# Performance work log

Measured on AMD Instinct MI355X. Metric: run time of the kernel, lower is better.

Reference implementation:

```python
import jax, jax.numpy as jnp
import numpy as np

D_MODEL, D_INNER, D_STATE, DT_RANK, D_CONV = 768, 1536, 16, 48, 4
B, L = 2, 2048


def setup_inputs() -> dict:
    key = jax.random.key(0)
    ks = jax.random.split(key, 8)
    s = 0.02
    return {
        "x": jax.random.normal(ks[0], (B, L, D_MODEL), jnp.float32),
        "norm_w": jnp.ones((D_MODEL,), jnp.float32),
        "in_proj_w": jax.random.normal(ks[1], (2 * D_INNER, D_MODEL), jnp.float32) * s,
        "conv_w": jax.random.normal(ks[2], (D_INNER, 1, D_CONV), jnp.float32) * s,
        "conv_b": jnp.zeros((D_INNER,), jnp.float32),
        "x_proj_w": jax.random.normal(ks[3], (DT_RANK + 2 * D_STATE, D_INNER), jnp.float32) * s,
        "dt_proj_w": jax.random.normal(ks[4], (D_INNER, DT_RANK), jnp.float32) * s,
        "dt_proj_b": jax.random.normal(ks[5], (D_INNER,), jnp.float32) * s,
        "A_log": jnp.broadcast_to(jnp.log(jnp.arange(1, D_STATE + 1, dtype=jnp.float32)), (D_INNER, D_STATE)).copy(),
        "D": jnp.ones((D_INNER,), jnp.float32),
        "out_proj_w": jax.random.normal(ks[6], (D_MODEL, D_INNER), jnp.float32) * s,
    }


def _mamba_block(x, norm_w, in_proj_w, conv_w, conv_b, x_proj_w,
                 dt_proj_w, dt_proj_b, A_log, D, out_proj_w):
    residual = x
    # RMSNorm
    h = x * jax.lax.rsqrt(jnp.mean(x * x, axis=-1, keepdims=True) + 1e-5) * norm_w
    # in_proj -> chunk into (hs, gate)
    xz = jnp.einsum('bld,ed->ble', h, in_proj_w)          # [B,L,2*Di]
    xh, z = jnp.split(xz, 2, axis=-1)                     # each [B,L,Di]
    # causal depthwise conv1d (kernel D_CONV) + SiLU
    xt = jnp.transpose(xh, (0, 2, 1))                     # [B,Di,L]
    xt = jnp.pad(xt, ((0, 0), (0, 0), (D_CONV - 1, 0)))
    xc = jax.lax.conv_general_dilated(xt, conv_w, (1,), 'VALID',
                                      feature_group_count=D_INNER)
    xc = jax.nn.silu(xc + conv_b[None, :, None])
    xc = jnp.transpose(xc, (0, 2, 1))                     # [B,L,Di]
    # x_proj -> (dt, B, C)
    proj = jnp.einsum('bld,ed->ble', xc, x_proj_w)        # [B,L,dt_rank+2N]
    dt, Bm, Cm = jnp.split(proj, [DT_RANK, DT_RANK + D_STATE], axis=-1)
    delta = jax.nn.softplus(jnp.einsum('blr,dr->bld', dt, dt_proj_w) + dt_proj_b)  # [B,L,Di]
    A = -jnp.exp(A_log)                                   # [Di,N]
    dA = jnp.exp(delta[..., None] * A)                    # [B,L,Di,N]
    dBx = delta[..., None] * Bm[:, :, None, :] * xc[..., None]  # [B,L,Di,N]
    # selective scan over the sequence axis
    def step(hst, inp):
        dA_t, dBx_t, C_t = inp                            # [B,Di,N],[B,Di,N],[B,N]
        hst = dA_t * hst + dBx_t
        y = jnp.einsum('bdn,bn->bd', hst, C_t)
        return hst, y
    h0 = jnp.zeros((x.shape[0], D_INNER, D_STATE), x.dtype)
    _, ys = jax.lax.scan(step, h0, (jnp.moveaxis(dA, 1, 0),
                                    jnp.moveaxis(dBx, 1, 0),
                                    jnp.moveaxis(Cm, 1, 0)))
    y = jnp.moveaxis(ys, 0, 1)                            # [B,L,Di]
    y = y + xc * D                                        # skip connection D
    y = y * jax.nn.silu(z)                                # gate
    out = jnp.einsum('bld,ed->ble', y, out_proj_w)        # [B,L,Dm]
    return residual + out, residual


def reference(x, norm_w, in_proj_w, conv_w, conv_b, x_proj_w,
              dt_proj_w, dt_proj_b, A_log, D, out_proj_w):
    return _mamba_block(x, norm_w, in_proj_w, conv_w, conv_b, x_proj_w,
                        dt_proj_w, dt_proj_b, A_log, D, out_proj_w)
```

## Files before the change

kernel.cpp:

```cpp
#include <hip/hip_runtime.h>
#include <cstdint>
#include <cstddef>

typedef __bf16 bf16_t;
typedef __bf16 bf16x8 __attribute__((ext_vector_type(8)));
typedef float  f32x4  __attribute__((ext_vector_type(4)));

#define D_MODEL 768
#define D_INNER 1536
#define D_STATE 16
#define DT_RANK 48
#define NB      2
#define SEQ     2048
#define NTOK    (NB*SEQ)
#define XPROJ_N (DT_RANK + 2*D_STATE)
#define LC      32
#define NCHUNK  (SEQ/LC)
#define XP_KS   4
#define XP_KC   (D_INNER/XP_KS)

#define N_INW (2*D_INNER*D_MODEL)
#define N_XPW (XPROJ_N*D_INNER)
#define N_DTW (D_INNER*DT_RANK)
#define N_OPW (D_MODEL*D_INNER)
#define N_CVT (N_INW+N_XPW+N_DTW+N_OPW)
#define CVT_BLOCKS (N_CVT/1024)

typedef __attribute__((address_space(1))) void gvoid_t;
typedef __attribute__((address_space(3))) void lvoid_t;
__device__ __forceinline__ void g2lds16(const bf16_t* g, bf16_t* l) {
    __builtin_amdgcn_global_load_lds((gvoid_t*)g, (lvoid_t*)l, 16, 0, 0);
}

__global__ __launch_bounds__(256)
void prep_kernel(const float* __restrict__ in_proj_w, bf16_t* __restrict__ w_in,
                 const float* __restrict__ x_proj_w,  bf16_t* __restrict__ w_xp,
                 const float* __restrict__ dt_proj_w, bf16_t* __restrict__ w_dt,
                 const float* __restrict__ out_proj_w,bf16_t* __restrict__ w_op,
                 const float* __restrict__ x, const float* __restrict__ norm_w,
                 bf16_t* __restrict__ h) {
    const int blk = blockIdx.x;
    const int tid = threadIdx.x;
    if (blk < CVT_BLOCKS) {
        int off = (blk * 256 + tid) * 4;
        const float* s; bf16_t* d;
        if (off < N_INW) { s = in_proj_w + off; d = w_in + off; }
        else if ((off -= N_INW) < N_XPW) { s = x_proj_w + off; d = w_xp + off; }
        else if ((off -= N_XPW) < N_DTW) { s = dt_proj_w + off; d = w_dt + off; }
        else { off -= N_DTW; s = out_proj_w + off; d = w_op + off; }
        float4 v = *(const float4*)s;
        d[0] = (bf16_t)v.x; d[1] = (bf16_t)v.y;
        d[2] = (bf16_t)v.z; d[3] = (bf16_t)v.w;
        return;
    }
    int t = blk - CVT_BLOCKS;
    const float* xr = x + (size_t)t * D_MODEL;
    float v[3];
    float ss = 0.f;
#pragma unroll
    for (int i = 0; i < 3; i++) { v[i] = xr[tid + 256*i]; ss += v[i]*v[i]; }
#pragma unroll
    for (int off = 32; off >= 1; off >>= 1) ss += __shfl_down(ss, off);
    __shared__ float red[4];
    int lane = tid & 63, wv = tid >> 6;
    if (lane == 0) red[wv] = ss;
    __syncthreads();
    float tot = red[0] + red[1] + red[2] + red[3];
    float r = rsqrtf(tot * (1.f/(float)D_MODEL) + 1e-5f);
#pragma unroll
    for (int i = 0; i < 3; i++)
        h[(size_t)t*D_MODEL + tid + 256*i] = (bf16_t)(v[i] * r * norm_w[tid + 256*i]);
}

__global__ __launch_bounds__(256)
void gemm_nt128(const bf16_t* __restrict__ A, int lda,
                const bf16_t* __restrict__ B, int ldb,
                bf16_t* __restrict__ C, int ldc, int K) {
    __shared__ __align__(16) bf16_t As[2][128*32];
    __shared__ __align__(16) bf16_t Bs[2][128*32];
    const int tid = threadIdx.x;
    const int wave = tid >> 6, lane = tid & 63;
    const int quad = lane >> 4, l16 = lane & 15;
    const int m0 = blockIdx.x * 128, n0 = blockIdx.y * 128;
    const int wr = (wave >> 1) * 64, wc = (wave & 1) * 64;

    const int s0 = tid, s1 = tid + 256;
    const int r0 = s0 >> 2, q0 = ((s0 & 3) ^ ((r0 >> 1) & 3)) << 3;
    const int r1 = s1 >> 2, q1 = ((s1 & 3) ^ ((r1 >> 1) & 3)) << 3;

    const bf16_t* Ar0 = A + (size_t)(m0 + r0)*lda + q0;
    const bf16_t* Ar1 = A + (size_t)(m0 + r1)*lda + q1;
    const bf16_t* Br0 = B + (size_t)(n0 + r0)*ldb + q0;
    const bf16_t* Br1 = B + (size_t)(n0 + r1)*ldb + q1;

    f32x4 acc[4][4] = {};
    const int nit = K >> 5;

    g2lds16(Ar0, &As[0][wave*512]);
    g2lds16(Ar1, &As[0][wave*512 + 2048]);
    g2lds16(Br0, &Bs[0][wave*512]);
    g2lds16(Br1, &Bs[0][wave*512 + 2048]);

    for (int it = 0; it < nit; it++) {
        __syncthreads();
        if (it + 1 < nit) {
            int k = (it + 1) << 5;
            int nb = (it + 1) & 1;
            g2lds16(Ar0 + k, &As[nb][wave*512]);
            g2lds16(Ar1 + k, &As[nb][wave*512 + 2048]);
            g2lds16(Br0 + k, &Bs[nb][wave*512]);
            g2lds16(Br1 + k, &Bs[nb][wave*512 + 2048]);
        }
        const int buf = it & 1;
        bf16x8 af[4], bfr[4];
#pragma unroll
        for (int i = 0; i < 4; i++) {
            int rr = wr + i*16 + l16;
            af[i] = *(const bf16x8*)&As[buf][rr*32 + ((quad ^ ((rr >> 1) & 3)) << 3)];
        }
#pragma unroll
        for (int j = 0; j < 4; j++) {
            int rr = wc + j*16 + l16;
            bfr[j] = *(const bf16x8*)&Bs[buf][rr*32 + ((quad ^ ((rr >> 1) & 3)) << 3)];
        }
#pragma unroll
        for (int i = 0; i < 4; i++)
#pragma unroll
            for (int j = 0; j < 4; j++)
                acc[i][j] = __builtin_amdgcn_mfma_f32_16x16x32_bf16(af[i], bfr[j], acc[i][j], 0, 0, 0);
    }

#pragma unroll
    for (int i = 0; i < 4; i++)
#pragma unroll
        for (int j = 0; j < 4; j++) {
            int n = n0 + wc + j*16 + l16;
#pragma unroll
            for (int rr = 0; rr < 4; rr++) {
                int m = m0 + wr + i*16 + quad*4 + rr;
                C[(size_t)m * ldc + n] = (bf16_t)acc[i][j][rr];
            }
        }
}

__global__ __launch_bounds__(256)
void gemm_op(const bf16_t* __restrict__ A, const bf16_t* __restrict__ B,
             float* __restrict__ C, const float* __restrict__ resid,
             float* __restrict__ resid_out) {
    __shared__ __align__(16) bf16_t As[2][128*32];
    __shared__ __align__(16) bf16_t Bs[2][64*32];
    const int tid = threadIdx.x;
    const int wave = tid >> 6, lane = tid & 63;
    const int quad = lane >> 4, l16 = lane & 15;
    const int m0 = blockIdx.x * 128, n0 = blockIdx.y * 64;
    const int wr = (wave >> 1) * 64, wc = (wave & 1) * 32;

    const int s0 = tid, s1 = tid + 256;
    const int r0 = s0 >> 2, q0 = ((s0 & 3) ^ ((r0 >> 1) & 3)) << 3;
    const int r1 = s1 >> 2, q1 = ((s1 & 3) ^ ((r1 >> 1) & 3)) << 3;
    const int rB = tid >> 2, qB = (((tid & 3) ^ ((rB >> 1) & 3)) << 3);

    const bf16_t* Ar0 = A + (size_t)(m0 + r0)*D_INNER + q0;
    const bf16_t* Ar1 = A + (size_t)(m0 + r1)*D_INNER + q1;
    const bf16_t* Brp = B + (size_t)(n0 + rB)*D_INNER + qB;

    f32x4 acc[4][2] = {};
    const int nit = D_INNER >> 5;

    g2lds16(Ar0, &As[0][wave*512]);
    g2lds16(Ar1, &As[0][wave*512 + 2048]);
    g2lds16(Brp, &Bs[0][wave*512]);

    for (int it = 0; it < nit; it++) {
        __syncthreads();
        if (it + 1 < nit) {
            int k = (it + 1) << 5;
            int nb = (it + 1) & 1;
            g2lds16(Ar0 + k, &As[nb][wave*512]);
            g2lds16(Ar1 + k, &As[nb][wave*512 + 2048]);
            g2lds16(Brp + k, &Bs[nb][wave*512]);
        }
        const int buf = it & 1;
        bf16x8 af[4], bfr[2];
#pragma unroll
        for (int i = 0; i < 4; i++) {
            int rr = wr + i*16 + l16;
            af[i] = *(const bf16x8*)&As[buf][rr*32 + ((quad ^ ((rr >> 1) & 3)) << 3)];
        }
#pragma unroll
        for (int j = 0; j < 2; j++) {
            int rr = wc + j*16 + l16;
            bfr[j] = *(const bf16x8*)&Bs[buf][rr*32 + ((quad ^ ((rr >> 1) & 3)) << 3)];
        }
#pragma unroll
        for (int i = 0; i < 4; i++)
#pragma unroll
            for (int j = 0; j < 2; j++)
                acc[i][j] = __builtin_amdgcn_mfma_f32_16x16x32_bf16(af[i], bfr[j], acc[i][j], 0, 0, 0);
    }

#pragma unroll
    for (int i = 0; i < 4; i++)
#pragma unroll
        for (int j = 0; j < 2; j++) {
            int n = n0 + wc + j*16 + l16;
#pragma unroll
            for (int rr = 0; rr < 4; rr++) {
                int m = m0 + wr + i*16 + quad*4 + rr;
                size_t idx = (size_t)m * D_MODEL + n;
                float rx = resid[idx];
                C[idx] = acc[i][j][rr] + rx;
                resid_out[idx] = rx;
            }
        }
}

__global__ __launch_bounds__(256)
void gemm_xp(const bf16_t* __restrict__ A, const bf16_t* __restrict__ B,
             float* __restrict__ pbuf) {
    __shared__ __align__(16) bf16_t As[64*32];
    __shared__ __align__(16) bf16_t Bs[64*32];
    const int tid = threadIdx.x;
    const int m0 = blockIdx.x * 64, n0 = blockIdx.y * 64, kbase = blockIdx.z * XP_KC;
    const int r  = tid >> 2, p8 = (tid & 3) << 3;
    const int q8 = (((tid & 3) ^ ((r >> 1) & 3)) << 3);
    const int wave = tid >> 6, lane = tid & 63;
    const int quad = lane >> 4, l16 = lane & 15;

    f32x4 acc[4] = {{0.f,0.f,0.f,0.f},{0.f,0.f,0.f,0.f},
                    {0.f,0.f,0.f,0.f},{0.f,0.f,0.f,0.f}};

    for (int k0 = 0; k0 < XP_KC; k0 += 32) {
        int gk = kbase + k0 + q8;
        uint4 va = *(const uint4*)(A + (size_t)(m0 + r) * D_INNER + gk);
        *(uint4*)&As[r*32 + p8] = va;
        uint4 vb = {0u,0u,0u,0u};
        int nr = n0 + r;
        if (nr < XPROJ_N)
            vb = *(const uint4*)(B + (size_t)nr * D_INNER + gk);
        *(uint4*)&Bs[r*32 + p8] = vb;

        __syncthreads();
        int ra = wave*16 + l16;
        bf16x8 af = *(const bf16x8*)&As[ra*32 + ((quad ^ ((ra >> 1) & 3)) << 3)];
#pragma unroll
        for (int nt = 0; nt < 4; nt++) {
            int rb = nt*16 + l16;
            bf16x8 bfg = *(const bf16x8*)&Bs[rb*32 + ((quad ^ ((rb >> 1) & 3)) << 3)];
            acc[nt] = __builtin_amdgcn_mfma_f32_16x16x32_bf16(af, bfg, acc[nt], 0, 0, 0);
        }
        __syncthreads();
    }

#pragma unroll
    for (int nt = 0; nt < 4; nt++) {
        int n = n0 + nt*16 + l16;
        if (n >= XPROJ_N) continue;
#pragma unroll
        for (int rr = 0; rr < 4; rr++) {
            int m = m0 + wave*16 + quad*4 + rr;
            pbuf[((size_t)blockIdx.z * NTOK + m) * XPROJ_N + n] = acc[nt][rr];
        }
    }
}

__global__ __launch_bounds__(256)
void xp_reduce_kernel(const float* __restrict__ pbuf, bf16_t* __restrict__ proj) {
    int i = blockIdx.x * 256 + threadIdx.x;
    if (i >= NTOK * XPROJ_N) return;
    float s = 0.f;
#pragma unroll
    for (int z = 0; z < XP_KS; z++)
        s += pbuf[(size_t)z * NTOK * XPROJ_N + i];
    proj[i] = (bf16_t)s;
}

__global__ __launch_bounds__(256)
void gemm_dt(const bf16_t* __restrict__ A, const bf16_t* __restrict__ B,
             bf16_t* __restrict__ C, const float* __restrict__ bias) {
    __shared__ __align__(16) bf16_t As[64*32];
    __shared__ __align__(16) bf16_t Bs[64*32];
    const int tid = threadIdx.x;
    const int m0 = blockIdx.x * 64, n0 = blockIdx.y * 64;
    const int r  = tid >> 2, p8 = (tid & 3) << 3;
    const int q8 = (((tid & 3) ^ ((r >> 1) & 3)) << 3);
    const int wave = tid >> 6, lane = tid & 63;
    const int quad = lane >> 4, l16 = lane & 15;

    f32x4 acc[4] = {{0.f,0.f,0.f,0.f},{0.f,0.f,0.f,0.f},
                    {0.f,0.f,0.f,0.f},{0.f,0.f,0.f,0.f}};

    for (int k0 = 0; k0 < DT_RANK; k0 += 32) {
        int gk = k0 + q8;
        uint4 va = {0u,0u,0u,0u};
        if (gk + 8 <= DT_RANK)
            va = *(const uint4*)(A + (size_t)(m0 + r) * XPROJ_N + gk);
        *(uint4*)&As[r*32 + p8] = va;
        uint4 vb = {0u,0u,0u,0u};
        if (gk + 8 <= DT_RANK)
            vb = *(const uint4*)(B + (size_t)(n0 + r) * DT_RANK + gk);
        *(uint4*)&Bs[r*32 + p8] = vb;

        __syncthreads();
        int ra = wave*16 + l16;
        bf16x8 af = *(const bf16x8*)&As[ra*32 + ((quad ^ ((ra >> 1) & 3)) << 3)];
#pragma unroll
        for (int nt = 0; nt < 4; nt++) {
            int rb = nt*16 + l16;
            bf16x8 bfg = *(const bf16x8*)&Bs[rb*32 + ((quad ^ ((rb >> 1) & 3)) << 3)];
            acc[nt] = __builtin_amdgcn_mfma_f32_16x16x32_bf16(af, bfg, acc[nt], 0, 0, 0);
        }
        __syncthreads();
    }

#pragma unroll
    for (int nt = 0; nt < 4; nt++) {
        int n = n0 + nt*16 + l16;
#pragma unroll
        for (int rr = 0; rr < 4; rr++) {
            int m = m0 + wave*16 + quad*4 + rr;
            float u = acc[nt][rr] + bias[n];
            float sp = (u > 20.f) ? u : log1pf(__expf(u));
            C[(size_t)m * D_INNER + n] = (bf16_t)sp;
        }
    }
}

__global__ __launch_bounds__(192)
void conv_silu_kernel(const bf16_t* __restrict__ xz,
                      const float* __restrict__ cw,
                      const float* __restrict__ cb,
                      bf16_t* __restrict__ xc) {
    const int t = blockIdx.x;
    const int l = t & (SEQ - 1);
    const int d = threadIdx.x * 8;

    float cwf[32];
#pragma unroll
    for (int q = 0; q < 8; q++)
        *(float4*)&cwf[q*4] = *(const float4*)&cw[d*4 + q*4];

    float acc[8];
    {
        float4 c0 = *(const float4*)&cb[d];
        float4 c1 = *(const float4*)&cb[d+4];
        acc[0]=c0.x; acc[1]=c0.y; acc[2]=c0.z; acc[3]=c0.w;
        acc[4]=c1.x; acc[5]=c1.y; acc[6]=c1.z; acc[7]=c1.w;
    }
#pragma unroll
    for (int k = 0; k < 4; k++) {
        if (l - 3 + k >= 0) {
            bf16x8 v = *(const bf16x8*)&xz[(size_t)(t - 3 + k) * (2*D_INNER) + d];
#pragma unroll
            for (int i = 0; i < 8; i++)
                acc[i] += (float)v[i] * cwf[i*4 + k];
        }
    }
    bf16x8 o;
#pragma unroll
    for (int i = 0; i < 8; i++) {
        float s = acc[i] / (1.f + __expf(-acc[i]));
        o[i] = (bf16_t)s;
    }
    *(bf16x8*)&xc[(size_t)t * D_INNER + d] = o;
}

__global__ __launch_bounds__(256)
void scan_part1(const bf16_t* __restrict__ delta,
                const bf16_t* __restrict__ xc,
                const bf16_t* __restrict__ proj,
                const float* __restrict__ A_log,
                float* __restrict__ chunk_h, float* __restrict__ chunk_P) {
    const int tid = threadIdx.x;
    const int d = blockIdx.x * 256 + tid;
    const int c = blockIdx.y;
    const int b = blockIdx.z;
    __shared__ float Bs[LC][D_STATE];
    for (int i = tid; i < LC*D_STATE; i += 256) {
        int l = i >> 4, n = i & 15;
        size_t t = (size_t)b*SEQ + (size_t)c*LC + l;
        Bs[l][n] = (float)proj[t*XPROJ_N + DT_RANK + n];
    }
    __syncthreads();
    float Av2[D_STATE];
#pragma unroll
    for (int n = 0; n < D_STATE; n++)
        Av2[n] = -__expf(A_log[d*D_STATE + n]) * 1.44269504f;
    float s[D_STATE];
#pragma unroll
    for (int n = 0; n < D_STATE; n++) s[n] = 0.f;
    float sdv = 0.f;
    const size_t tbase = (size_t)b*SEQ + (size_t)c*LC;
    for (int l = 0; l < LC; l++) {
        size_t t = tbase + l;
        float dv  = (float)delta[t*D_INNER + d];
        float xcv = (float)xc[t*D_INNER + d];
        float dx = dv * xcv;
        sdv += dv;
#pragma unroll
        for (int n = 0; n < D_STATE; n++) {
            float a = __builtin_amdgcn_exp2f(dv * Av2[n]);
            s[n] = a * s[n] + dx * Bs[l][n];
        }
    }
    size_t base = (((size_t)b*NCHUNK + c)*D_INNER + d)*D_STATE;
#pragma unroll
    for (int n = 0; n < D_STATE; n++) {
        chunk_h[base + n] = s[n];
        chunk_P[base + n] = __builtin_amdgcn_exp2f(Av2[n] * sdv);
    }
}

__global__ __launch_bounds__(256)
void scan_part2(float* __restrict__ chunk_h, const float* __restrict__ chunk_P) {
    int gid = blockIdx.x * 256 + threadIdx.x;
    int b  = gid / (D_INNER * D_STATE);
    int dn = gid - b * (D_INNER * D_STATE);
    float H = 0.f;
    for (int c = 0; c < NCHUNK; c++) {
        size_t idx = ((size_t)b*NCHUNK + c)*D_INNER*D_STATE + dn;
        float S = chunk_h[idx];
        float P = chunk_P[idx];
        chunk_h[idx] = H;
        H = P * H + S;
    }
}

__global__ __launch_bounds__(256)
void scan_part3(const bf16_t* __restrict__ delta,
                const bf16_t* __restrict__ xc,
                const bf16_t* __restrict__ proj,
                const bf16_t* __restrict__ xz,
                const float* __restrict__ A_log,
                const float* __restrict__ Dw,
                const float* __restrict__ chunk_h,
                bf16_t* __restrict__ y) {
    const int tid = threadIdx.x;
    const int d = blockIdx.x * 256 + tid;
    const int c = blockIdx.y;
    const int b = blockIdx.z;
    __shared__ float Bs[LC][D_STATE];
    __shared__ float Cs[LC][D_STATE];
    for (int i = tid; i < LC*D_STATE; i += 256) {
        int l = i >> 4, n = i & 15;
        size_t t = (size_t)b*SEQ + (size_t)c*LC + l;
        Bs[l][n] = (float)proj[t*XPROJ_N + DT_RANK + n];
        Cs[l][n] = (float)proj[t*XPROJ_N + DT_RANK + D_STATE + n];
    }
    __syncthreads();
    float Av2[D_STATE];
#pragma unroll
    for (int n = 0; n < D_STATE; n++)
        Av2[n] = -__expf(A_log[d*D_STATE + n]) * 1.44269504f;
    const float Dv = Dw[d];
    float s[D_STATE];
    size_t base = (((size_t)b*NCHUNK + c)*D_INNER + d)*D_STATE;
#pragma unroll
    for (int n = 0; n < D_STATE; n++) s[n] = chunk_h[base + n];
    const size_t tbase = (size_t)b*SEQ + (size_t)c*LC;
    for (int l = 0; l < LC; l++) {
        size_t t = tbase + l;
        float dv  = (float)delta[t*D_INNER + d];
        float xcv = (float)xc[t*D_INNER + d];
        float dx = dv * xcv;
        float acc = 0.f;
#pragma unroll
        for (int n = 0; n < D_STATE; n++) {
            float a = __builtin_amdgcn_exp2f(dv * Av2[n]);
            s[n] = a * s[n] + dx * Bs[l][n];
            acc += s[n] * Cs[l][n];
        }
        float zf = (float)xz[t*(2*D_INNER) + D_INNER + d];
        float g = zf / (1.f + __expf(-zf));
        y[t*D_INNER + d] = (bf16_t)((acc + xcv * Dv) * g);
    }
}

extern "C" void kernel_launch(void* const* d_in, const int* in_sizes, int n_in,
                              void* d_out, int out_size, void* d_ws, size_t ws_size,
                              hipStream_t stream) {
    const float* x          = (const float*)d_in[0];
    const float* norm_w     = (const float*)d_in[1];
    const float* in_proj_w  = (const float*)d_in[2];
    const float* conv_w     = (const float*)d_in[3];
    const float* conv_b     = (const float*)d_in[4];
    const float* x_proj_w   = (const float*)d_in[5];
    const float* dt_proj_w  = (const float*)d_in[6];
    const float* dt_proj_b  = (const float*)d_in[7];
    const float* A_log      = (const float*)d_in[8];
    const float* Dw         = (const float*)d_in[9];
    const float* out_proj_w = (const float*)d_in[10];

    float* out0 = (float*)d_out;
    float* out1 = out0 + (size_t)NTOK * D_MODEL;

    const size_t n_chunkst = (size_t)NB*NCHUNK*D_INNER*D_STATE;

    char* ws = (char*)d_ws;
    bf16_t* w_in  = (bf16_t*)ws;  ws += (size_t)N_INW * sizeof(bf16_t);
    bf16_t* w_xp  = (bf16_t*)ws;  ws += (size_t)N_XPW * sizeof(bf16_t);
    bf16_t* w_dt  = (bf16_t*)ws;  ws += (size_t)N_DTW * sizeof(bf16_t);
    bf16_t* w_op  = (bf16_t*)ws;  ws += (size_t)N_OPW * sizeof(bf16_t);
    bf16_t* h     = (bf16_t*)ws;  ws += (size_t)NTOK * D_MODEL   * sizeof(bf16_t);
    bf16_t* xz    = (bf16_t*)ws;  ws += (size_t)NTOK * 2*D_INNER * sizeof(bf16_t);
    bf16_t* xc    = (bf16_t*)ws;  ws += (size_t)NTOK * D_INNER   * sizeof(bf16_t);
    bf16_t* proj  = (bf16_t*)ws;  ws += (size_t)NTOK * XPROJ_N   * sizeof(bf16_t);
    bf16_t* delta = (bf16_t*)ws;  ws += (size_t)NTOK * D_INNER   * sizeof(bf16_t);
    bf16_t* y     = (bf16_t*)ws;  ws += (size_t)NTOK * D_INNER   * sizeof(bf16_t);
    float*  ch    = (float*)ws;   ws += n_chunkst * sizeof(float);
    float*  cP    = (float*)ws;   ws += n_chunkst * sizeof(float);
    float*  xppart= (float*)ws;   ws += (size_t)XP_KS * NTOK * XPROJ_N * sizeof(float);

    prep_kernel<<<CVT_BLOCKS + NTOK, 256, 0, stream>>>(
        in_proj_w, w_in, x_proj_w, w_xp, dt_proj_w, w_dt, out_proj_w, w_op,
        x, norm_w, h);
    gemm_nt128<<<dim3(NTOK/128, (2*D_INNER)/128), 256, 0, stream>>>(
        h, D_MODEL, w_in, D_MODEL, xz, 2*D_INNER, D_MODEL);
    conv_silu_kernel<<<NTOK, 192, 0, stream>>>(xz, conv_w, conv_b, xc);
    gemm_xp<<<dim3(NTOK/64, 2, XP_KS), 256, 0, stream>>>(xc, w_xp, xppart);
    xp_reduce_kernel<<<(NTOK*XPROJ_N + 255)/256, 256, 0, stream>>>(xppart, proj);
    gemm_dt<<<dim3(NTOK/64, D_INNER/64), 256, 0, stream>>>(proj, w_dt, delta, dt_proj_b);
    scan_part1<<<dim3(D_INNER/256, NCHUNK, NB), 256, 0, stream>>>(
        delta, xc, proj, A_log, ch, cP);
    scan_part2<<<(int)((size_t)NB*D_INNER*D_STATE/256), 256, 0, stream>>>(ch, cP);
    scan_part3<<<dim3(D_INNER/256, NCHUNK, NB), 256, 0, stream>>>(
        delta, xc, proj, xz, A_log, Dw, ch, y);
    gemm_op<<<dim3(NTOK/128, D_MODEL/64), 256, 0, stream>>>(
        y, w_op, out0, x, out1);
}
```

Measured before the change: 291.3 us.

## Fuse chunked scan into cooperative kernel and replace x_proj split-K reduce with atomics

Merges the three scan kernels into one cooperative kernel that uses grid-wide syncs, keeping delta/xc packed in registers between phases and recomputing chunk decay from per-chunk delta sums. This removes the chunk_P buffer and the reloads of delta/xc. The x_proj split-K now accumulates with fp32 atomics into a buffer zeroed in prep_kernel, which drops the separate reduce kernel. gemm_dt and the scan read fp32 proj directly. The costs are two grid syncs, extra register pressure from the 32-entry pack array, non-deterministic atomic summation, and a cooperative launch that needs all 768 blocks to be co-resident.

```diff
diff --git a/kernel.cpp b/kernel.cpp
--- a/kernel.cpp
+++ b/kernel.cpp
@@ -1,6 +1,9 @@
 #include <hip/hip_runtime.h>
+#include <hip/hip_cooperative_groups.h>
 #include <cstdint>
 #include <cstddef>
+
+namespace cg = cooperative_groups;
 
 typedef __bf16 bf16_t;
 typedef __bf16 bf16x8 __attribute__((ext_vector_type(8)));
@@ -25,6 +28,7 @@
 #define N_OPW (D_MODEL*D_INNER)
 #define N_CVT (N_INW+N_XPW+N_DTW+N_OPW)
 #define CVT_BLOCKS (N_CVT/1024)
+#define ZERO_BLOCKS ((NTOK*XPROJ_N)/1024)
 
 typedef __attribute__((address_space(1))) void gvoid_t;
 typedef __attribute__((address_space(3))) void lvoid_t;
@@ -38,7 +42,7 @@
                  const float* __restrict__ dt_proj_w, bf16_t* __restrict__ w_dt,
                  const float* __restrict__ out_proj_w,bf16_t* __restrict__ w_op,
                  const float* __restrict__ x, const float* __restrict__ norm_w,
-                 bf16_t* __restrict__ h) {
+                 bf16_t* __restrict__ h, float* __restrict__ projf) {
     const int blk = blockIdx.x;
     const int tid = threadIdx.x;
     if (blk < CVT_BLOCKS) {
@@ -53,6 +57,12 @@
         d[2] = (bf16_t)v.z; d[3] = (bf16_t)v.w;
         return;
     }
+    if (blk >= CVT_BLOCKS + NTOK) {
+        int i = (blk - CVT_BLOCKS - NTOK) * 1024 + tid * 4;
+        float4 z = {0.f, 0.f, 0.f, 0.f};
+        *(float4*)&projf[i] = z;
+        return;
+    }
     int t = blk - CVT_BLOCKS;
     const float* xr = x + (size_t)t * D_MODEL;
     float v[3];
@@ -217,7 +227,7 @@
 
 __global__ __launch_bounds__(256)
 void gemm_xp(const bf16_t* __restrict__ A, const bf16_t* __restrict__ B,
-             float* __restrict__ pbuf) {
+             float* __restrict__ projf) {
     __shared__ __align__(16) bf16_t As[64*32];
     __shared__ __align__(16) bf16_t Bs[64*32];
     const int tid = threadIdx.x;
@@ -259,24 +269,13 @@
 #pragma unroll
         for (int rr = 0; rr < 4; rr++) {
             int m = m0 + wave*16 + quad*4 + rr;
-            pbuf[((size_t)blockIdx.z * NTOK + m) * XPROJ_N + n] = acc[nt][rr];
+            atomicAdd(&projf[(size_t)m * XPROJ_N + n], acc[nt][rr]);
         }
     }
 }
 
 __global__ __launch_bounds__(256)
-void xp_reduce_kernel(const float* __restrict__ pbuf, bf16_t* __restrict__ proj) {
-    int i = blockIdx.x * 256 + threadIdx.x;
-    if (i >= NTOK * XPROJ_N) return;
-    float s = 0.f;
-#pragma unroll
-    for (int z = 0; z < XP_KS; z++)
-        s += pbuf[(size_t)z * NTOK * XPROJ_N + i];
-    proj[i] = (bf16_t)s;
-}
-
-__global__ __launch_bounds__(256)
-void gemm_dt(const bf16_t* __restrict__ A, const bf16_t* __restrict__ B,
+void gemm_dt(const float* __restrict__ projf, const bf16_t* __restrict__ B,
              bf16_t* __restrict__ C, const float* __restrict__ bias) {
     __shared__ __align__(16) bf16_t As[64*32];
     __shared__ __align__(16) bf16_t Bs[64*32];
@@ -292,10 +291,15 @@
 
     for (int k0 = 0; k0 < DT_RANK; k0 += 32) {
         int gk = k0 + q8;
-        uint4 va = {0u,0u,0u,0u};
-        if (gk + 8 <= DT_RANK)
-            va = *(const uint4*)(A + (size_t)(m0 + r) * XPROJ_N + gk);
-        *(uint4*)&As[r*32 + p8] = va;
+        bf16x8 av = {};
+        if (gk + 8 <= DT_RANK) {
+            const float* ap = projf + (size_t)(m0 + r) * XPROJ_N + gk;
+            float4 f0 = *(const float4*)ap;
+            float4 f1 = *(const float4*)(ap + 4);
+            av[0]=(bf16_t)f0.x; av[1]=(bf16_t)f0.y; av[2]=(bf16_t)f0.z; av[3]=(bf16_t)f0.w;
+            av[4]=(bf16_t)f1.x; av[5]=(bf16_t)f1.y; av[6]=(bf16_t)f1.z; av[7]=(bf16_t)f1.w;
+        }
+        *(bf16x8*)&As[r*32 + p8] = av;
         uint4 vb = {0u,0u,0u,0u};
         if (gk + 8 <= DT_RANK)
             vb = *(const uint4*)(B + (size_t)(n0 + r) * DT_RANK + gk);
@@ -366,75 +370,16 @@
 }
 
 __global__ __launch_bounds__(256)
-void scan_part1(const bf16_t* __restrict__ delta,
+void scan_fused(const bf16_t* __restrict__ delta,
                 const bf16_t* __restrict__ xc,
-                const bf16_t* __restrict__ proj,
-                const float* __restrict__ A_log,
-                float* __restrict__ chunk_h, float* __restrict__ chunk_P) {
-    const int tid = threadIdx.x;
-    const int d = blockIdx.x * 256 + tid;
-    const int c = blockIdx.y;
-    const int b = blockIdx.z;
-    __shared__ float Bs[LC][D_STATE];
-    for (int i = tid; i < LC*D_STATE; i += 256) {
-        int l = i >> 4, n = i & 15;
-        size_t t = (size_t)b*SEQ + (size_t)c*LC + l;
-        Bs[l][n] = (float)proj[t*XPROJ_N + DT_RANK + n];
-    }
-    __syncthreads();
-    float Av2[D_STATE];
-#pragma unroll
-    for (int n = 0; n < D_STATE; n++)
-        Av2[n] = -__expf(A_log[d*D_STATE + n]) * 1.44269504f;
-    float s[D_STATE];
-#pragma unroll
-    for (int n = 0; n < D_STATE; n++) s[n] = 0.f;
-    float sdv = 0.f;
-    const size_t tbase = (size_t)b*SEQ + (size_t)c*LC;
-    for (int l = 0; l < LC; l++) {
-        size_t t = tbase + l;
-        float dv  = (float)delta[t*D_INNER + d];
-        float xcv = (float)xc[t*D_INNER + d];
-        float dx = dv * xcv;
-        sdv += dv;
-#pragma unroll
-        for (int n = 0; n < D_STATE; n++) {
-            float a = __builtin_amdgcn_exp2f(dv * Av2[n]);
-            s[n] = a * s[n] + dx * Bs[l][n];
-        }
-    }
-    size_t base = (((size_t)b*NCHUNK + c)*D_INNER + d)*D_STATE;
-#pragma unroll
-    for (int n = 0; n < D_STATE; n++) {
-        chunk_h[base + n] = s[n];
-        chunk_P[base + n] = __builtin_amdgcn_exp2f(Av2[n] * sdv);
-    }
-}
-
-__global__ __launch_bounds__(256)
-void scan_part2(float* __restrict__ chunk_h, const float* __restrict__ chunk_P) {
-    int gid = blockIdx.x * 256 + threadIdx.x;
-    int b  = gid / (D_INNER * D_STATE);
-    int dn = gid - b * (D_INNER * D_STATE);
-    float H = 0.f;
-    for (int c = 0; c < NCHUNK; c++) {
-        size_t idx = ((size_t)b*NCHUNK + c)*D_INNER*D_STATE + dn;
-        float S = chunk_h[idx];
-        float P = chunk_P[idx];
-        chunk_h[idx] = H;
-        H = P * H + S;
-    }
-}
-
-__global__ __launch_bounds__(256)
-void scan_part3(const bf16_t* __restrict__ delta,
-                const bf16_t* __restrict__ xc,
-                const bf16_t* __restrict__ proj,
+                const float* __restrict__ projf,
                 const bf16_t* __restrict__ xz,
                 const float* __restrict__ A_log,
                 const float* __restrict__ Dw,
-                const float* __restrict__ chunk_h,
+                float* __restrict__ Sbuf,
+                float* __restrict__ sdvbuf,
                 bf16_t* __restrict__ y) {
+    cg::grid_group grid = cg::this_grid();
     const int tid = threadIdx.x;
     const int d = blockIdx.x * 256 + tid;
     const int c = blockIdx.y;
@@ -444,25 +389,75 @@
     for (int i = tid; i < LC*D_STATE; i += 256) {
         int l = i >> 4, n = i & 15;
         size_t t = (size_t)b*SEQ + (size_t)c*LC + l;
-        Bs[l][n] = (float)proj[t*XPROJ_N + DT_RANK + n];
-        Cs[l][n] = (float)proj[t*XPROJ_N + DT_RANK + D_STATE + n];
-    }
-    __syncthreads();
+        Bs[l][n] = projf[t*XPROJ_N + DT_RANK + n];
+        Cs[l][n] = projf[t*XPROJ_N + DT_RANK + D_STATE + n];
+    }
     float Av2[D_STATE];
 #pragma unroll
     for (int n = 0; n < D_STATE; n++)
         Av2[n] = -__expf(A_log[d*D_STATE + n]) * 1.44269504f;
-    const float Dv = Dw[d];
+    __syncthreads();
+
+    const unsigned short* dpu = (const unsigned short*)delta;
+    const unsigned short* xpu = (const unsigned short*)xc;
+    const size_t tbase = (size_t)b*SEQ + (size_t)c*LC;
+    unsigned pack[LC];
     float s[D_STATE];
-    size_t base = (((size_t)b*NCHUNK + c)*D_INNER + d)*D_STATE;
-#pragma unroll
-    for (int n = 0; n < D_STATE; n++) s[n] = chunk_h[base + n];
-    const size_t tbase = (size_t)b*SEQ + (size_t)c*LC;
+#pragma unroll
+    for (int n = 0; n < D_STATE; n++) s[n] = 0.f;
+    float sdv = 0.f;
     for (int l = 0; l < LC; l++) {
         size_t t = tbase + l;
-        float dv  = (float)delta[t*D_INNER + d];
-        float xcv = (float)xc[t*D_INNER + d];
-        float dx = dv * xcv;
+        unsigned dvu = dpu[t*D_INNER + d];
+        unsigned xcu = xpu[t*D_INNER + d];
+        pack[l] = (xcu << 16) | dvu;
+        float dv  = __uint_as_float(dvu << 16);
+        float xcf = __uint_as_float(pack[l] & 0xFFFF0000u);
+        float dx = dv * xcf;
+        sdv += dv;
+#pragma unroll
+        for (int n = 0; n < D_STATE; n++) {
+            float a = __builtin_amdgcn_exp2f(dv * Av2[n]);
+            s[n] = a * s[n] + dx * Bs[l][n];
+        }
+    }
+    const size_t base = (((size_t)b*NCHUNK + c)*D_INNER + d)*D_STATE;
+#pragma unroll
+    for (int n = 0; n < D_STATE; n++) Sbuf[base + n] = s[n];
+    sdvbuf[((size_t)b*NCHUNK + c)*D_INNER + d] = sdv;
+
+    __threadfence();
+    grid.sync();
+
+    {
+        unsigned rank = (unsigned)grid.thread_rank();
+        if (rank < (unsigned)(NB * D_INNER * D_STATE)) {
+            int b2 = rank / (D_INNER * D_STATE);
+            int dn = rank - b2 * (D_INNER * D_STATE);
+            int d2 = dn >> 4;
+            float Avc = -__expf(A_log[dn]) * 1.44269504f;
+            float H = 0.f;
+            for (int c2 = 0; c2 < NCHUNK; c2++) {
+                size_t idx = ((size_t)b2*NCHUNK + c2)*D_INNER*D_STATE + dn;
+                float S  = Sbuf[idx];
+                float sv = sdvbuf[((size_t)b2*NCHUNK + c2)*D_INNER + d2];
+                Sbuf[idx] = H;
+                H = __builtin_amdgcn_exp2f(Avc * sv) * H + S;
+            }
+        }
+    }
+
+    __threadfence();
+    grid.sync();
+
+#pragma unroll
+    for (int n = 0; n < D_STATE; n++) s[n] = Sbuf[base + n];
+    const float Dv = Dw[d];
+    for (int l = 0; l < LC; l++) {
+        size_t t = tbase + l;
+        float dv  = __uint_as_float(pack[l] << 16);
+        float xcf = __uint_as_float(pack[l] & 0xFFFF0000u);
+        float dx = dv * xcf;
         float acc = 0.f;
 #pragma unroll
         for (int n = 0; n < D_STATE; n++) {
@@ -472,7 +467,7 @@
         }
         float zf = (float)xz[t*(2*D_INNER) + D_INNER + d];
         float g = zf / (1.f + __expf(-zf));
-        y[t*D_INNER + d] = (bf16_t)((acc + xcv * Dv) * g);
+        y[t*D_INNER + d] = (bf16_t)((acc + xcf * Dv) * g);
     }
 }
 
@@ -504,27 +499,29 @@
     bf16_t* h     = (bf16_t*)ws;  ws += (size_t)NTOK * D_MODEL   * sizeof(bf16_t);
     bf16_t* xz    = (bf16_t*)ws;  ws += (size_t)NTOK * 2*D_INNER * sizeof(bf16_t);
     bf16_t* xc    = (bf16_t*)ws;  ws += (size_t)NTOK * D_INNER   * sizeof(bf16_t);
-    bf16_t* proj  = (bf16_t*)ws;  ws += (size_t)NTOK * XPROJ_N   * sizeof(bf16_t);
+    float*  projf = (float*)ws;   ws += (size_t)NTOK * XPROJ_N   * sizeof(float);
     bf16_t* delta = (bf16_t*)ws;  ws += (size_t)NTOK * D_INNER   * sizeof(bf16_t);
     bf16_t* y     = (bf16_t*)ws;  ws += (size_t)NTOK * D_INNER   * sizeof(bf16_t);
-    float*  ch    = (float*)ws;   ws += n_chunkst * sizeof(float);
-    float*  cP    = (float*)ws;   ws += n_chunkst * sizeof(float);
-    float*  xppart= (float*)ws;   ws += (size_t)XP_KS * NTOK * XPROJ_N * sizeof(float);
-
-    prep_kernel<<<CVT_BLOCKS + NTOK, 256, 0, stream>>>(
+    float*  Sbuf  = (float*)ws;   ws += n_chunkst * sizeof(float);
+    float*  sdvb  = (float*)ws;   ws += (size_t)NB*NCHUNK*D_INNER * sizeof(float);
+
+    prep_kernel<<<CVT_BLOCKS + NTOK + ZERO_BLOCKS, 256, 0, stream>>>(
         in_proj_w, w_in, x_proj_w, w_xp, dt_proj_w, w_dt, out_proj_w, w_op,
-        x, norm_w, h);
+        x, norm_w, h, projf);
     gemm_nt128<<<dim3(NTOK/128, (2*D_INNER)/128), 256, 0, stream>>>(
         h, D_MODEL, w_in, D_MODEL, xz, 2*D_INNER, D_MODEL);
     conv_silu_kernel<<<NTOK, 192, 0, stream>>>(xz, conv_w, conv_b, xc);
-    gemm_xp<<<dim3(NTOK/64, 2, XP_KS), 256, 0, stream>>>(xc, w_xp, xppart);
-    xp_reduce_kernel<<<(NTOK*XPROJ_N + 255)/256, 256, 0, stream>>>(xppart, proj);
-    gemm_dt<<<dim3(NTOK/64, D_INNER/64), 256, 0, stream>>>(proj, w_dt, delta, dt_proj_b);
-    scan_part1<<<dim3(D_INNER/256, NCHUNK, NB), 256, 0, stream>>>(
-        delta, xc, proj, A_log, ch, cP);
-    scan_part2<<<(int)((size_t)NB*D_INNER*D_STATE/256), 256, 0, stream>>>(ch, cP);
-    scan_part3<<<dim3(D_INNER/256, NCHUNK, NB), 256, 0, stream>>>(
-        delta, xc, proj, xz, A_log, Dw, ch, y);
+    gemm_xp<<<dim3(NTOK/64, 2, XP_KS), 256, 0, stream>>>(xc, w_xp, projf);
+    gemm_dt<<<dim3(NTOK/64, D_INNER/64), 256, 0, stream>>>(projf, w_dt, delta, dt_proj_b);
+    {
+        const bf16_t* a0 = delta; const bf16_t* a1 = xc; const float* a2 = projf;
+        const bf16_t* a3 = xz; const float* a4 = A_log; const float* a5 = Dw;
+        float* a6 = Sbuf; float* a7 = sdvb; bf16_t* a8 = y;
+        void* args[] = {&a0, &a1, &a2, &a3, &a4, &a5, &a6, &a7, &a8};
+        hipLaunchCooperativeKernel((void*)scan_fused,
+                                   dim3(D_INNER/256, NCHUNK, NB), dim3(256),
+                                   args, 0, stream);
+    }
     gemm_op<<<dim3(NTOK/128, D_MODEL/64), 256, 0, stream>>>(
         y, w_op, out0, x, out1);
 }
```

Result: slower. 627.2 us (+115.3%).
